# Kernel tuning notes

Measured on AMD Instinct MI355X. Metric: run time of the kernel, lower is better.

The kernel has to match this reference:

```python
import jax, jax.numpy as jnp
import numpy as np

B, S, D = 16, 2048, 512

def setup_inputs() -> dict:
    key = jax.random.key(0)
    k0, k1, k2, k3 = jax.random.split(key, 4)
    scale = 1.0 / np.sqrt(D)
    return {
        "inputs": jax.random.normal(k0, (B, S, D), dtype=jnp.float32),
        "W_q": jax.random.normal(k1, (D, D), dtype=jnp.float32) * scale,
        "W_k": jax.random.normal(k2, (D, D), dtype=jnp.float32) * scale,
        "W_v": jax.random.normal(k3, (D, D), dtype=jnp.float32) * scale,
    }

def reference(inputs, W_q, W_k, W_v):
    # Q/K/V projections: [B,S,D]
    q = jnp.einsum('bsd,de->bse', inputs, W_q)
    k = jnp.einsum('bsd,de->bse', inputs, W_k)
    v = jnp.einsum('bsd,de->bse', inputs, W_v)
    d_k = jnp.asarray(q.shape[-1], dtype=q.dtype)
    scores = jnp.einsum('bqd,bkd->bqk', q, k) / jnp.sqrt(d_k)  # [B,S,S]
    attn = jax.nn.softmax(scores, axis=-1)
    out = jnp.einsum('bqk,bkd->bqd', attn, v)  # [B,S,D]
    return jnp.sum(out, axis=1)  # sum-pool over seq -> [B,D]
```

## Files before the change

kernel.cpp:

```cpp
#include <hip/hip_runtime.h>
#include <hip/hip_bf16.h>


#define S_LEN 2048
#define D_DIM 512
#define BATCH 16

typedef short bf16x8 __attribute__((ext_vector_type(8)));
typedef float f32x4 __attribute__((ext_vector_type(4)));

typedef __attribute__((address_space(3))) void lds_void_t;
typedef const __attribute__((address_space(1))) void gbl_void_t;

__device__ __forceinline__ void async_copy16(const void* g, void* l) {
  __builtin_amdgcn_global_load_lds((gbl_void_t*)g, (lds_void_t*)l, 16, 0, 0);
}

__device__ __forceinline__ unsigned short f2bf(float f) {
  unsigned u = __float_as_uint(f);
  u += 0x7fff + ((u >> 16) & 1);
  return (unsigned short)(u >> 16);
}
__device__ __forceinline__ float bf2f(unsigned short h) {
  return __uint_as_float((unsigned)h << 16);
}

#if __has_builtin(__builtin_amdgcn_cvt_pk_fp8_f32) && __has_builtin(__builtin_amdgcn_cvt_f32_fp8)
#define HAVE_FP8CVT 1
#else
#define HAVE_FP8CVT 0
#endif

__device__ __forceinline__ unsigned enc8(float x) {
  unsigned u = __float_as_uint(x);
  unsigned t = (u + 0x7FFFFu + ((u >> 20) & 1u)) >> 20;
  int b = (int)t - 0x3C0;
  b = b < 0 ? 0 : (b > 127 ? 127 : b);
  return (unsigned)b;
}
__device__ __forceinline__ float dec8(unsigned b) {
  return b ? __uint_as_float((b + 0x3C0u) << 20) : 0.0f;
}

__device__ __forceinline__ unsigned pack4_fp8(float e0, float e1, float e2, float e3) {
#if HAVE_FP8CVT
  unsigned dw = (unsigned)__builtin_amdgcn_cvt_pk_fp8_f32(e0, e1, 0, false);
  dw = (unsigned)__builtin_amdgcn_cvt_pk_fp8_f32(e2, e3, (int)dw, true);
  return dw;
#else
  return enc8(e0) | (enc8(e1) << 8) | (enc8(e2) << 16) | (enc8(e3) << 24);
#endif
}

__device__ __forceinline__ void gemm_core_nt(
    const unsigned short* __restrict__ A, long lda,
    const unsigned short* __restrict__ B, long ldb,
    int K, unsigned short* As, unsigned short* Bs, f32x4 acc[4][4])
{
  const int tid  = threadIdx.x;
  const int lane = tid & 63;
  const int w    = tid >> 6;
  const int wm   = w >> 1, wn = w & 1;
  const int r16  = lane & 15;
  const int kq   = lane >> 4;

  const int j0 = w * 64 + lane;
  const int j1 = (w + 4) * 64 + lane;
  const int r0 = j0 >> 2, cc0 = (((j0 & 3) - (r0 >> 1)) & 3);
  const int r1 = j1 >> 2, cc1 = (((j1 & 3) - (r1 >> 1)) & 3);

  const long a0 = (long)r0 * lda + cc0 * 8;
  const long a1 = (long)r1 * lda + cc1 * 8;
  const long b0 = (long)r0 * ldb + cc0 * 8;
  const long b1 = (long)r1 * ldb + cc1 * 8;

  int aoff[4], boff[4];
#pragma unroll
  for (int mt = 0; mt < 4; ++mt) {
    const int row = wm * 64 + mt * 16 + r16;
    aoff[mt] = row * 32 + (((row >> 1) + kq) & 3) * 8;
  }
#pragma unroll
  for (int nt = 0; nt < 4; ++nt) {
    const int row = wn * 64 + nt * 16 + r16;
    boff[nt] = row * 32 + (((row >> 1) + kq) & 3) * 8;
  }

  for (int k0 = 0; k0 < K; k0 += 32) {
    __syncthreads();
    async_copy16(A + a0 + k0, (char*)As + (w    ) * 1024);
    async_copy16(A + a1 + k0, (char*)As + (w + 4) * 1024);
    async_copy16(B + b0 + k0, (char*)Bs + (w    ) * 1024);
    async_copy16(B + b1 + k0, (char*)Bs + (w + 4) * 1024);
    __syncthreads();

    bf16x8 af[4], bg[4];
#pragma unroll
    for (int mt = 0; mt < 4; ++mt) af[mt] = *(const bf16x8*)&As[aoff[mt]];
#pragma unroll
    for (int nt = 0; nt < 4; ++nt) bg[nt] = *(const bf16x8*)&Bs[boff[nt]];
#pragma unroll
    for (int mt = 0; mt < 4; ++mt)
#pragma unroll
      for (int nt = 0; nt < 4; ++nt)
        acc[mt][nt] = __builtin_amdgcn_mfma_f32_16x16x32_bf16(af[mt], bg[nt], acc[mt][nt], 0, 0, 0);
  }
}

__global__ __launch_bounds__(256) void k_prep(
    const float* __restrict__ X, const float* __restrict__ Wq, const float* __restrict__ Wk,
    unsigned short* __restrict__ Xbf, unsigned short* __restrict__ Wqb,
    unsigned short* __restrict__ Wkb, float* __restrict__ zp, float* __restrict__ out)
{
  const int blk = blockIdx.x;
  if (blk < 16384) {
    int i = (blk * 256 + threadIdx.x) * 4;
    float4 v = *(const float4*)(X + i);
    ushort4 o;
    o.x = f2bf(v.x); o.y = f2bf(v.y); o.z = f2bf(v.z); o.w = f2bf(v.w);
    *(ushort4*)(Xbf + i) = o;
  } else if (blk < 16896) {
    const int b2 = blk - 16384;
    const float* s = (b2 < 256) ? Wq : Wk;
    unsigned short* d = (b2 < 256) ? Wqb : Wkb;
    int i = ((b2 & 255) * 256 + threadIdx.x) * 4;
    float4 v = *(const float4*)(s + i);
    ushort4 o;
    o.x = f2bf(v.x); o.y = f2bf(v.y); o.z = f2bf(v.z); o.w = f2bf(v.w);
    *(ushort4*)(d + i) = o;
  } else {
    int i = (blk - 16896) * 256 + threadIdx.x;
    if (i < 73728) zp[i] = 0.0f;
    else out[i - 73728] = 0.0f;
  }
}

__global__ __launch_bounds__(256) void k_mt(
    const unsigned short* __restrict__ A, const unsigned short* __restrict__ B,
    unsigned short* __restrict__ C, float scale)
{
  __shared__ alignas(16) unsigned short As[64 * 32];
  __shared__ alignas(16) unsigned short Bs[64 * 32];
  f32x4 acc[2][2] = {};
  const int tid = threadIdx.x, lane = tid & 63, w = tid >> 6;
  const int wm = w >> 1, wn = w & 1, r16 = lane & 15, kq = lane >> 4;
  const long a0row = (long)blockIdx.y * 64, b0row = (long)blockIdx.x * 64;

  const int prow = tid >> 2, pslot = tid & 3, pc = (pslot - prow) & 3;
  const long asrc = (a0row + prow) * 512 + pc * 8;
  const long bsrc = (b0row + prow) * 512 + pc * 8;

  int aoff[2], boff[2];
#pragma unroll
  for (int t = 0; t < 2; ++t) {
    const int m = wm * 32 + t * 16 + r16;
    aoff[t] = m * 32 + ((m + kq) & 3) * 8;
    const int n = wn * 32 + t * 16 + r16;
    boff[t] = n * 32 + ((n + kq) & 3) * 8;
  }

  for (int k0 = 0; k0 < 512; k0 += 32) {
    __syncthreads();
    async_copy16(A + asrc + k0, (char*)As + w * 1024);
    async_copy16(B + bsrc + k0, (char*)Bs + w * 1024);
    __syncthreads();
    bf16x8 af[2], bg[2];
#pragma unroll
    for (int t = 0; t < 2; ++t) { af[t] = *(const bf16x8*)&As[aoff[t]]; bg[t] = *(const bf16x8*)&Bs[boff[t]]; }
#pragma unroll
    for (int mt = 0; mt < 2; ++mt)
#pragma unroll
      for (int nt = 0; nt < 2; ++nt)
        acc[mt][nt] = __builtin_amdgcn_mfma_f32_16x16x32_bf16(af[mt], bg[nt], acc[mt][nt], 0, 0, 0);
  }

  const int quad = lane >> 4;
#pragma unroll
  for (int mt = 0; mt < 2; ++mt)
#pragma unroll
    for (int nt = 0; nt < 2; ++nt)
#pragma unroll
      for (int r = 0; r < 4; ++r)
        C[(a0row + wm * 32 + mt * 16 + quad * 4 + r) * 512 + b0row + wn * 32 + nt * 16 + r16]
            = f2bf(acc[mt][nt][r] * scale);
}

__global__ __launch_bounds__(256) void k_gemm_bf16out(
    const unsigned short* __restrict__ A, long lda,
    const unsigned short* __restrict__ B, long ldb, int K,
    unsigned short* __restrict__ C, long ldc, float scale)
{
  __shared__ alignas(16) unsigned short As[128 * 32];
  __shared__ alignas(16) unsigned short Bs[128 * 32];
  f32x4 acc[4][4] = {};
  const long am0 = (long)blockIdx.y * 128;
  const long bn0 = (long)blockIdx.x * 128;
  gemm_core_nt(A + am0 * lda, lda, B + bn0 * ldb, ldb, K, As, Bs, acc);

  const int lane = threadIdx.x & 63;
  const int w = threadIdx.x >> 6, wm = w >> 1, wn = w & 1;
  const long row0 = am0 + wm * 64 + (lane >> 4) * 4;
  const long col0 = bn0 + wn * 64 + (lane & 15);
#pragma unroll
  for (int mt = 0; mt < 4; ++mt)
#pragma unroll
    for (int nt = 0; nt < 4; ++nt)
#pragma unroll
      for (int r = 0; r < 4; ++r)
        C[(row0 + mt * 16 + r) * ldc + col0 + nt * 16] = f2bf(acc[mt][nt][r] * scale);
}

union SMemAE {
  struct { unsigned short As[128 * 32]; unsigned short Bs[128 * 32]; } s;
  unsigned E32[128 * 36];
};

__global__ __launch_bounds__(256) void k_passAE(
    const unsigned short* __restrict__ Ybf, const unsigned short* __restrict__ Xbf,
    float* __restrict__ lrow, unsigned* __restrict__ E)
{
  __shared__ SMemAE sm;
  f32x4 acc[4][4] = {};
  const int b = blockIdx.z, qt = blockIdx.y, kt = blockIdx.x;
  const long q0 = (long)qt * 128;
  const long n0 = (long)kt * 128;
  gemm_core_nt(Ybf + ((long)b * S_LEN + q0) * D_DIM, D_DIM,
               Xbf + ((long)b * S_LEN + n0) * D_DIM, D_DIM, D_DIM,
               sm.s.As, sm.s.Bs, acc);

  const int lane = threadIdx.x & 63;
  const int w = threadIdx.x >> 6, wm = w >> 1, wn = w & 1;
  const int r16 = lane & 15, quad = lane >> 4;

  __syncthreads();

#pragma unroll
  for (int mt = 0; mt < 4; ++mt) {
    float rs[4] = {0.f, 0.f, 0.f, 0.f};
#pragma unroll
    for (int nt = 0; nt < 4; ++nt) {
      float ev[4];
#pragma unroll
      for (int r = 0; r < 4; ++r) {
        ev[r] = __builtin_amdgcn_exp2f(acc[mt][nt][r]);
        rs[r] += ev[r];
      }
      const int col = wn * 64 + nt * 16 + r16;
      const int r4  = wm * 16 + mt * 4 + quad;
      sm.E32[col * 36 + r4] = pack4_fp8(ev[0], ev[1], ev[2], ev[3]);
    }
#pragma unroll
    for (int r = 0; r < 4; ++r) {
      float s = rs[r];
      s += __shfl_xor(s, 1, 64);
      s += __shfl_xor(s, 2, 64);
      s += __shfl_xor(s, 4, 64);
      s += __shfl_xor(s, 8, 64);
      if (r16 == 0)
        atomicAdd(&lrow[(long)b * S_LEN + q0 + wm * 64 + mt * 16 + quad * 4 + r], s);
    }
  }
  __syncthreads();

  unsigned* Eg = E + (((long)(b * 16 + qt)) * 16 + kt) * 4096;
  const int t = threadIdx.x;
#pragma unroll
  for (int p = 0; p < 4; ++p) {
    const int n = p * 256 + t;
    const int col = n >> 3, hj = n & 7;
    uint4 v = *(const uint4*)&sm.E32[col * 36 + hj * 4];
    *(uint4*)(Eg + n * 4) = v;
  }
}

__global__ __launch_bounds__(256) void k_wsum(
    const unsigned* __restrict__ E, const float* __restrict__ lrow,
    float* __restrict__ wcol)
{
  __shared__ float rl[512];
  const int kt = blockIdx.x, qq = blockIdx.y, b = blockIdx.z;
  const int tid = threadIdx.x;
  {
    const float* lp = lrow + (long)b * S_LEN + qq * 512;
    rl[tid]       = 1.0f / lp[tid];
    rl[tid + 256] = 1.0f / lp[tid + 256];
  }
  __syncthreads();
  const int col = tid & 127, qsel = tid >> 7;
  float acc = 0.0f;
#pragma unroll
  for (int qt2 = 0; qt2 < 2; ++qt2) {
    const int qtl = qsel * 2 + qt2;
    const int qt = qq * 4 + qtl;
    const unsigned* Ep = E + (((long)(b * 16 + qt)) * 16 + kt) * 4096 + col * 32;
    const float* rlq = rl + qtl * 128;
#pragma unroll
    for (int j = 0; j < 8; ++j) {
      uint4 v = *(const uint4*)(Ep + j * 4);
      const unsigned dws[4] = {v.x, v.y, v.z, v.w};
#pragma unroll
      for (int i = 0; i < 4; ++i) {
        const unsigned dv = dws[i];
        const float* r = rlq + j * 16 + i * 4;
#if HAVE_FP8CVT
        acc += __builtin_amdgcn_cvt_f32_fp8((int)dv, 0) * r[0];
        acc += __builtin_amdgcn_cvt_f32_fp8((int)dv, 1) * r[1];
        acc += __builtin_amdgcn_cvt_f32_fp8((int)dv, 2) * r[2];
        acc += __builtin_amdgcn_cvt_f32_fp8((int)dv, 3) * r[3];
#else
        acc += dec8( dv        & 0xFFu) * r[0];
        acc += dec8((dv >>  8) & 0xFFu) * r[1];
        acc += dec8((dv >> 16) & 0xFFu) * r[2];
        acc += dec8((dv >> 24)        ) * r[3];
#endif
      }
    }
  }
  atomicAdd(&wcol[(long)b * S_LEN + kt * 128 + col], acc);
}

__global__ __launch_bounds__(256) void k_passA(
    const unsigned short* __restrict__ Ybf, const unsigned short* __restrict__ Xbf,
    float* __restrict__ lrow)
{
  __shared__ alignas(16) unsigned short As[128 * 32];
  __shared__ alignas(16) unsigned short Bs[128 * 32];
  f32x4 acc[4][4] = {};
  const int b = blockIdx.z;
  const long q0 = (long)blockIdx.y * 128;
  const long n0 = (long)blockIdx.x * 128;
  gemm_core_nt(Ybf + ((long)b * S_LEN + q0) * D_DIM, D_DIM,
               Xbf + ((long)b * S_LEN + n0) * D_DIM, D_DIM, D_DIM, As, Bs, acc);

  const int lane = threadIdx.x & 63;
  const int w = threadIdx.x >> 6, wm = w >> 1;
#pragma unroll
  for (int mt = 0; mt < 4; ++mt) {
#pragma unroll
    for (int r = 0; r < 4; ++r) {
      float s = 0.0f;
#pragma unroll
      for (int nt = 0; nt < 4; ++nt) s += __builtin_amdgcn_exp2f(acc[mt][nt][r]);
      s += __shfl_xor(s, 1, 64);
      s += __shfl_xor(s, 2, 64);
      s += __shfl_xor(s, 4, 64);
      s += __shfl_xor(s, 8, 64);
      if ((lane & 15) == 0)
        atomicAdd(&lrow[(long)b * S_LEN + q0 + wm * 64 + mt * 16 + (lane >> 4) * 4 + r], s);
    }
  }
}

__global__ __launch_bounds__(256) void k_passB(
    const unsigned short* __restrict__ Ybf, const unsigned short* __restrict__ Xbf,
    const float* __restrict__ lrow, float* __restrict__ wcol)
{
  __shared__ alignas(16) unsigned short As[128 * 32];
  __shared__ alignas(16) unsigned short Bs[128 * 32];
  f32x4 acc[4][4] = {};
  const int b = blockIdx.z;
  const long q0 = (long)blockIdx.y * 128;
  const long n0 = (long)blockIdx.x * 128;
  gemm_core_nt(Ybf + ((long)b * S_LEN + q0) * D_DIM, D_DIM,
               Xbf + ((long)b * S_LEN + n0) * D_DIM, D_DIM, D_DIM, As, Bs, acc);

  const int lane = threadIdx.x & 63;
  const int w = threadIdx.x >> 6, wm = w >> 1, wn = w & 1;
  float csv[4] = {0.0f, 0.0f, 0.0f, 0.0f};
#pragma unroll
  for (int mt = 0; mt < 4; ++mt) {
    const float4 lv = *(const float4*)&lrow[(long)b * S_LEN + q0 + wm * 64 + mt * 16 + (lane >> 4) * 4];
    const float rv[4] = {1.0f / lv.x, 1.0f / lv.y, 1.0f / lv.z, 1.0f / lv.w};
#pragma unroll
    for (int nt = 0; nt < 4; ++nt)
#pragma unroll
      for (int r = 0; r < 4; ++r)
        csv[nt] += __builtin_amdgcn_exp2f(acc[mt][nt][r]) * rv[r];
  }
#pragma unroll
  for (int nt = 0; nt < 4; ++nt) {
    csv[nt] += __shfl_xor(csv[nt], 16, 64);
    csv[nt] += __shfl_xor(csv[nt], 32, 64);
  }
  if (lane < 16) {
#pragma unroll
    for (int nt = 0; nt < 4; ++nt)
      atomicAdd(&wcol[(long)b * S_LEN + n0 + wn * 64 + nt * 16 + lane], csv[nt]);
  }
}

__global__ __launch_bounds__(256) void k_t(
    const unsigned short* __restrict__ Xbf, const float* __restrict__ wcol,
    float* __restrict__ tvec)
{
  const int b = blockIdx.z;
  const int d = blockIdx.x * 256 + threadIdx.x;
  const int k0 = blockIdx.y * 64;
  const unsigned short* Xp = Xbf + ((long)b * S_LEN + k0) * D_DIM + d;
  const float* wp = wcol + (long)b * S_LEN + k0;
  float acc = 0.0f;
#pragma unroll 8
  for (int k = 0; k < 64; ++k) acc += wp[k] * bf2f(Xp[(long)k * D_DIM]);
  atomicAdd(&tvec[b * D_DIM + d], acc);
}

__global__ __launch_bounds__(128) void k_out(
    const float* __restrict__ tvec, const float* __restrict__ Wv, float* __restrict__ out)
{
  __shared__ float tl[128];
  const int b = blockIdx.y;
  const int d0 = blockIdx.z * 128;
  const int e = blockIdx.x * 128 + threadIdx.x;
  tl[threadIdx.x] = tvec[b * D_DIM + d0 + threadIdx.x];
  __syncthreads();
  float acc = 0.0f;
#pragma unroll 8
  for (int d = 0; d < 128; ++d) acc += tl[d] * Wv[(long)(d0 + d) * D_DIM + e];
  atomicAdd(&out[b * D_DIM + e], acc);
}

extern "C" void kernel_launch(void* const* d_in, const int* in_sizes, int n_in,
                              void* d_out, int out_size, void* d_ws, size_t ws_size,
                              hipStream_t stream) {
  const float* X  = (const float*)d_in[0];
  const float* Wq = (const float*)d_in[1];
  const float* Wk = (const float*)d_in[2];
  const float* Wv = (const float*)d_in[3];
  float* out = (float*)d_out;

  char* ws = (char*)d_ws;
  unsigned short* Xbf = (unsigned short*)(ws);
  unsigned short* Ybf = (unsigned short*)(ws + 33554432);
  unsigned short* Mt  = (unsigned short*)(ws + 67108864);
  unsigned short* Wqb = (unsigned short*)(ws + 67633152);
  unsigned short* Wkb = (unsigned short*)(ws + 68157440);
  float* lrow = (float*)(ws + 68681728);
  float* wcol = (float*)(ws + 68812800);
  float* tvec = (float*)(ws + 68943872);
  unsigned* E = (unsigned*)(ws + 69206016);
  const bool bigws = ws_size >= (size_t)69206016 + (size_t)67108864;

  k_prep<<<17216, 256, 0, stream>>>(X, Wq, Wk, Xbf, Wqb, Wkb, lrow, out);

  const float scale = 1.4426950408889634f / 22.627416997969522f;
  k_mt<<<dim3(8, 8), 256, 0, stream>>>(Wkb, Wqb, Mt, scale);

  k_gemm_bf16out<<<dim3(4, 256), 256, 0, stream>>>(Xbf, 512, Mt, 512, 512, Ybf, 512, 1.0f);

  if (bigws) {
    k_passAE<<<dim3(16, 16, 16), 256, 0, stream>>>(Ybf, Xbf, lrow, E);
    k_wsum<<<dim3(16, 4, 16), 256, 0, stream>>>(E, lrow, wcol);
  } else {
    k_passA<<<dim3(16, 16, 16), 256, 0, stream>>>(Ybf, Xbf, lrow);
    k_passB<<<dim3(16, 16, 16), 256, 0, stream>>>(Ybf, Xbf, lrow, wcol);
  }

  k_t<<<dim3(2, 32, 16), 256, 0, stream>>>(Xbf, wcol, tvec);
  k_out<<<dim3(4, 16, 4), 128, 0, stream>>>(tvec, Wv, out);
}
```

Measured before the change: 272.3 us.

## Use 32x32x16 MFMA in score pass and replace tvec atomics with partials

The score GEMM in k_passAE moves from 16x16x32 MFMA tiles to 32x32x16 MFMA with a new LDS swizzle and fragment layout. The exp/row-sum epilogue is rewritten to match the 32x32 accumulator layout. This is meant to cut LDS fragment reads and instruction count per FLOP. Separately, k_t now writes per-chunk partial sums into a buffer that reuses the Ybf region, and k_out reduces them, which removes the float atomics and the tvec zeroing.

```diff
diff --git a/kernel.cpp b/kernel.cpp
--- a/kernel.cpp
+++ b/kernel.cpp
@@ -8,6 +8,7 @@
 
 typedef short bf16x8 __attribute__((ext_vector_type(8)));
 typedef float f32x4 __attribute__((ext_vector_type(4)));
+typedef float f32x16 __attribute__((ext_vector_type(16)));
 
 typedef __attribute__((address_space(3))) void lds_void_t;
 typedef const __attribute__((address_space(1))) void gbl_void_t;
@@ -104,6 +105,65 @@
 #pragma unroll
       for (int nt = 0; nt < 4; ++nt)
         acc[mt][nt] = __builtin_amdgcn_mfma_f32_16x16x32_bf16(af[mt], bg[nt], acc[mt][nt], 0, 0, 0);
+  }
+}
+
+__device__ __forceinline__ void gemm_core_nt32(
+    const unsigned short* __restrict__ A, long lda,
+    const unsigned short* __restrict__ B, long ldb,
+    int K, unsigned short* As, unsigned short* Bs, f32x16 acc2[2][2])
+{
+  const int tid  = threadIdx.x;
+  const int lane = tid & 63;
+  const int w    = tid >> 6;
+  const int wm   = w >> 1, wn = w & 1;
+  const int c32  = lane & 31;
+  const int g    = lane >> 5;
+
+  const int j0 = w * 64 + lane;
+  const int j1 = (w + 4) * 64 + lane;
+  const int r0 = j0 >> 2, cc0 = (((j0 & 3) - (r0 >> 1)) & 3);
+  const int r1 = j1 >> 2, cc1 = (((j1 & 3) - (r1 >> 1)) & 3);
+
+  const long a0 = (long)r0 * lda + cc0 * 8;
+  const long a1 = (long)r1 * lda + cc1 * 8;
+  const long b0 = (long)r0 * ldb + cc0 * 8;
+  const long b1 = (long)r1 * ldb + cc1 * 8;
+
+  int aoff[2][2], boff[2][2];
+#pragma unroll
+  for (int ks = 0; ks < 2; ++ks) {
+#pragma unroll
+    for (int t = 0; t < 2; ++t) {
+      const int m = wm * 64 + t * 32 + c32;
+      aoff[ks][t] = m * 32 + (((m >> 1) + ks * 2 + g) & 3) * 8;
+      const int n = wn * 64 + t * 32 + c32;
+      boff[ks][t] = n * 32 + (((n >> 1) + ks * 2 + g) & 3) * 8;
+    }
+  }
+
+  for (int k0 = 0; k0 < K; k0 += 32) {
+    __syncthreads();
+    async_copy16(A + a0 + k0, (char*)As + (w    ) * 1024);
+    async_copy16(A + a1 + k0, (char*)As + (w + 4) * 1024);
+    async_copy16(B + b0 + k0, (char*)Bs + (w    ) * 1024);
+    async_copy16(B + b1 + k0, (char*)Bs + (w + 4) * 1024);
+    __syncthreads();
+
+#pragma unroll
+    for (int ks = 0; ks < 2; ++ks) {
+      bf16x8 af[2], bg[2];
+#pragma unroll
+      for (int t = 0; t < 2; ++t) {
+        af[t] = *(const bf16x8*)&As[aoff[ks][t]];
+        bg[t] = *(const bf16x8*)&Bs[boff[ks][t]];
+      }
+#pragma unroll
+      for (int mt = 0; mt < 2; ++mt)
+#pragma unroll
+        for (int nt = 0; nt < 2; ++nt)
+          acc2[mt][nt] = __builtin_amdgcn_mfma_f32_32x32x16_bf16(af[mt], bg[nt], acc2[mt][nt], 0, 0, 0);
+    }
   }
 }
 
@@ -130,8 +190,8 @@
     *(ushort4*)(d + i) = o;
   } else {
     int i = (blk - 16896) * 256 + threadIdx.x;
-    if (i < 73728) zp[i] = 0.0f;
-    else out[i - 73728] = 0.0f;
+    if (i < 65536) zp[i] = 0.0f;
+    else out[i - 65536] = 0.0f;
   }
 }
 
@@ -220,44 +280,48 @@
     float* __restrict__ lrow, unsigned* __restrict__ E)
 {
   __shared__ SMemAE sm;
-  f32x4 acc[4][4] = {};
+  f32x16 acc2[2][2] = {};
   const int b = blockIdx.z, qt = blockIdx.y, kt = blockIdx.x;
   const long q0 = (long)qt * 128;
   const long n0 = (long)kt * 128;
-  gemm_core_nt(Ybf + ((long)b * S_LEN + q0) * D_DIM, D_DIM,
-               Xbf + ((long)b * S_LEN + n0) * D_DIM, D_DIM, D_DIM,
-               sm.s.As, sm.s.Bs, acc);
+  gemm_core_nt32(Ybf + ((long)b * S_LEN + q0) * D_DIM, D_DIM,
+                 Xbf + ((long)b * S_LEN + n0) * D_DIM, D_DIM, D_DIM,
+                 sm.s.As, sm.s.Bs, acc2);
 
   const int lane = threadIdx.x & 63;
   const int w = threadIdx.x >> 6, wm = w >> 1, wn = w & 1;
-  const int r16 = lane & 15, quad = lane >> 4;
+  const int c32 = lane & 31, g = lane >> 5;
 
   __syncthreads();
 
 #pragma unroll
-  for (int mt = 0; mt < 4; ++mt) {
-    float rs[4] = {0.f, 0.f, 0.f, 0.f};
-#pragma unroll
-    for (int nt = 0; nt < 4; ++nt) {
-      float ev[4];
+  for (int mt = 0; mt < 2; ++mt) {
+#pragma unroll
+    for (int j = 0; j < 4; ++j) {
+      float rs[4] = {0.f, 0.f, 0.f, 0.f};
+#pragma unroll
+      for (int nt = 0; nt < 2; ++nt) {
+        float ev[4];
+#pragma unroll
+        for (int r = 0; r < 4; ++r) {
+          ev[r] = __builtin_amdgcn_exp2f(acc2[mt][nt][j * 4 + r]);
+          rs[r] += ev[r];
+        }
+        const int col = wn * 64 + nt * 32 + c32;
+        const int r4  = wm * 16 + mt * 8 + j * 2 + g;
+        sm.E32[col * 36 + r4] = pack4_fp8(ev[0], ev[1], ev[2], ev[3]);
+      }
 #pragma unroll
       for (int r = 0; r < 4; ++r) {
-        ev[r] = __builtin_amdgcn_exp2f(acc[mt][nt][r]);
-        rs[r] += ev[r];
+        float s = rs[r];
+        s += __shfl_xor(s, 1, 64);
+        s += __shfl_xor(s, 2, 64);
+        s += __shfl_xor(s, 4, 64);
+        s += __shfl_xor(s, 8, 64);
+        s += __shfl_xor(s, 16, 64);
+        if (c32 == 0)
+          atomicAdd(&lrow[(long)b * S_LEN + q0 + wm * 64 + mt * 32 + j * 8 + g * 4 + r], s);
       }
-      const int col = wn * 64 + nt * 16 + r16;
-      const int r4  = wm * 16 + mt * 4 + quad;
-      sm.E32[col * 36 + r4] = pack4_fp8(ev[0], ev[1], ev[2], ev[3]);
-    }
-#pragma unroll
-    for (int r = 0; r < 4; ++r) {
-      float s = rs[r];
-      s += __shfl_xor(s, 1, 64);
-      s += __shfl_xor(s, 2, 64);
-      s += __shfl_xor(s, 4, 64);
-      s += __shfl_xor(s, 8, 64);
-      if (r16 == 0)
-        atomicAdd(&lrow[(long)b * S_LEN + q0 + wm * 64 + mt * 16 + quad * 4 + r], s);
     }
   }
   __syncthreads();
@@ -391,27 +455,31 @@
 
 __global__ __launch_bounds__(256) void k_t(
     const unsigned short* __restrict__ Xbf, const float* __restrict__ wcol,
-    float* __restrict__ tvec)
-{
-  const int b = blockIdx.z;
+    float* __restrict__ tpart)
+{
+  const int b = blockIdx.z, kc = blockIdx.y;
   const int d = blockIdx.x * 256 + threadIdx.x;
-  const int k0 = blockIdx.y * 64;
+  const int k0 = kc * 128;
   const unsigned short* Xp = Xbf + ((long)b * S_LEN + k0) * D_DIM + d;
   const float* wp = wcol + (long)b * S_LEN + k0;
   float acc = 0.0f;
 #pragma unroll 8
-  for (int k = 0; k < 64; ++k) acc += wp[k] * bf2f(Xp[(long)k * D_DIM]);
-  atomicAdd(&tvec[b * D_DIM + d], acc);
+  for (int k = 0; k < 128; ++k) acc += wp[k] * bf2f(Xp[(long)k * D_DIM]);
+  tpart[((long)kc * BATCH + b) * D_DIM + d] = acc;
 }
 
 __global__ __launch_bounds__(128) void k_out(
-    const float* __restrict__ tvec, const float* __restrict__ Wv, float* __restrict__ out)
+    const float* __restrict__ tpart, const float* __restrict__ Wv, float* __restrict__ out)
 {
   __shared__ float tl[128];
   const int b = blockIdx.y;
   const int d0 = blockIdx.z * 128;
   const int e = blockIdx.x * 128 + threadIdx.x;
-  tl[threadIdx.x] = tvec[b * D_DIM + d0 + threadIdx.x];
+  float tv = 0.0f;
+#pragma unroll
+  for (int kc = 0; kc < 16; ++kc)
+    tv += tpart[((long)kc * BATCH + b) * D_DIM + d0 + threadIdx.x];
+  tl[threadIdx.x] = tv;
   __syncthreads();
   float acc = 0.0f;
 #pragma unroll 8
@@ -436,11 +504,11 @@
   unsigned short* Wkb = (unsigned short*)(ws + 68157440);
   float* lrow = (float*)(ws + 68681728);
   float* wcol = (float*)(ws + 68812800);
-  float* tvec = (float*)(ws + 68943872);
   unsigned* E = (unsigned*)(ws + 69206016);
+  float* tpart = (float*)(ws + 33554432);
   const bool bigws = ws_size >= (size_t)69206016 + (size_t)67108864;
 
-  k_prep<<<17216, 256, 0, stream>>>(X, Wq, Wk, Xbf, Wqb, Wkb, lrow, out);
+  k_prep<<<17184, 256, 0, stream>>>(X, Wq, Wk, Xbf, Wqb, Wkb, lrow, out);
 
   const float scale = 1.4426950408889634f / 22.627416997969522f;
   k_mt<<<dim3(8, 8), 256, 0, stream>>>(Wkb, Wqb, Mt, scale);
@@ -455,6 +523,6 @@
     k_passB<<<dim3(16, 16, 16), 256, 0, stream>>>(Ybf, Xbf, lrow, wcol);
   }
 
-  k_t<<<dim3(2, 32, 16), 256, 0, stream>>>(Xbf, wcol, tvec);
-  k_out<<<dim3(4, 16, 4), 128, 0, stream>>>(tvec, Wv, out);
-}
+  k_t<<<dim3(2, 16, 16), 256, 0, stream>>>(Xbf, wcol, tpart);
+  k_out<<<dim3(4, 16, 4), 128, 0, stream>>>(tpart, Wv, out);
+}
```

After: 308.7 us. +13.4%, slower.

## Remap GEMM blocks per XCD for L2 locality and replace atomics with partial sums

Applied to the files above, without the earlier changes.

Block indices in the Y-projection GEMM and the scores pass are remapped so that consecutive blocks dispatched to the same XCD share a batch or row panel, which should improve L2 reuse on the chiplet design. The t-vector reduction no longer uses atomics: each block writes vectorized partial sums into a scratch buffer, and the output kernel reduces the 64 partials itself. The prep kernel stops zeroing the old tvec. The scratch buffer reuses the Ybf workspace region, which is safe only because Ybf is dead by that point in the stream.

```diff
diff --git a/kernel.cpp b/kernel.cpp
--- a/kernel.cpp
+++ b/kernel.cpp
@@ -130,8 +130,8 @@
     *(ushort4*)(d + i) = o;
   } else {
     int i = (blk - 16896) * 256 + threadIdx.x;
-    if (i < 73728) zp[i] = 0.0f;
-    else out[i - 73728] = 0.0f;
+    if (i < 65536) zp[i] = 0.0f;
+    else out[i - 65536] = 0.0f;
   }
 }
 
@@ -185,17 +185,18 @@
             = f2bf(acc[mt][nt][r] * scale);
 }
 
-__global__ __launch_bounds__(256) void k_gemm_bf16out(
-    const unsigned short* __restrict__ A, long lda,
-    const unsigned short* __restrict__ B, long ldb, int K,
-    unsigned short* __restrict__ C, long ldc, float scale)
+__global__ __launch_bounds__(256) void k_ygemm(
+    const unsigned short* __restrict__ A, const unsigned short* __restrict__ Mt,
+    unsigned short* __restrict__ C)
 {
   __shared__ alignas(16) unsigned short As[128 * 32];
   __shared__ alignas(16) unsigned short Bs[128 * 32];
   f32x4 acc[4][4] = {};
-  const long am0 = (long)blockIdx.y * 128;
-  const long bn0 = (long)blockIdx.x * 128;
-  gemm_core_nt(A + am0 * lda, lda, B + bn0 * ldb, ldb, K, As, Bs, acc);
+  const int L = blockIdx.x + (blockIdx.y << 2);
+  const int xcd = L & 7, seq = L >> 3;
+  const long am0 = (long)(xcd * 32 + (seq >> 2)) * 128;
+  const long bn0 = (long)(seq & 3) * 128;
+  gemm_core_nt(A + am0 * 512, 512, Mt + bn0 * 512, 512, 512, As, Bs, acc);
 
   const int lane = threadIdx.x & 63;
   const int w = threadIdx.x >> 6, wm = w >> 1, wn = w & 1;
@@ -207,7 +208,7 @@
     for (int nt = 0; nt < 4; ++nt)
 #pragma unroll
       for (int r = 0; r < 4; ++r)
-        C[(row0 + mt * 16 + r) * ldc + col0 + nt * 16] = f2bf(acc[mt][nt][r] * scale);
+        C[(row0 + mt * 16 + r) * 512 + col0 + nt * 16] = f2bf(acc[mt][nt][r]);
 }
 
 union SMemAE {
@@ -221,7 +222,11 @@
 {
   __shared__ SMemAE sm;
   f32x4 acc[4][4] = {};
-  const int b = blockIdx.z, qt = blockIdx.y, kt = blockIdx.x;
+  const int L = blockIdx.x + (blockIdx.y << 4) + (blockIdx.z << 8);
+  const int xcd = L & 7, seq = L >> 3;
+  const int b  = xcd * 2 + (seq >> 8);
+  const int s2 = seq & 255;
+  const int qt = s2 >> 4, kt = s2 & 15;
   const long q0 = (long)qt * 128;
   const long n0 = (long)kt * 128;
   gemm_core_nt(Ybf + ((long)b * S_LEN + q0) * D_DIM, D_DIM,
@@ -391,27 +396,39 @@
 
 __global__ __launch_bounds__(256) void k_t(
     const unsigned short* __restrict__ Xbf, const float* __restrict__ wcol,
-    float* __restrict__ tvec)
-{
-  const int b = blockIdx.z;
-  const int d = blockIdx.x * 256 + threadIdx.x;
-  const int k0 = blockIdx.y * 64;
+    float* __restrict__ tpart)
+{
+  const int b = blockIdx.z, kc = blockIdx.y;
+  const int tid = threadIdx.x;
+  const int c4 = tid & 127, ksel = tid >> 7;
+  const int k0 = kc * 64 + ksel * 32;
+  const int d = c4 * 4;
   const unsigned short* Xp = Xbf + ((long)b * S_LEN + k0) * D_DIM + d;
   const float* wp = wcol + (long)b * S_LEN + k0;
-  float acc = 0.0f;
+  float a0 = 0, a1 = 0, a2 = 0, a3 = 0;
 #pragma unroll 8
-  for (int k = 0; k < 64; ++k) acc += wp[k] * bf2f(Xp[(long)k * D_DIM]);
-  atomicAdd(&tvec[b * D_DIM + d], acc);
+  for (int k = 0; k < 32; ++k) {
+    ushort4 xv = *(const ushort4*)(Xp + (long)k * D_DIM);
+    const float wv = wp[k];
+    a0 += wv * bf2f(xv.x); a1 += wv * bf2f(xv.y);
+    a2 += wv * bf2f(xv.z); a3 += wv * bf2f(xv.w);
+  }
+  float4 o; o.x = a0; o.y = a1; o.z = a2; o.w = a3;
+  *(float4*)&tpart[((long)(kc * 2 + ksel) * BATCH + b) * D_DIM + d] = o;
 }
 
 __global__ __launch_bounds__(128) void k_out(
-    const float* __restrict__ tvec, const float* __restrict__ Wv, float* __restrict__ out)
+    const float* __restrict__ tpart, const float* __restrict__ Wv, float* __restrict__ out)
 {
   __shared__ float tl[128];
   const int b = blockIdx.y;
   const int d0 = blockIdx.z * 128;
   const int e = blockIdx.x * 128 + threadIdx.x;
-  tl[threadIdx.x] = tvec[b * D_DIM + d0 + threadIdx.x];
+  float tv = 0.0f;
+#pragma unroll
+  for (int p = 0; p < 64; ++p)
+    tv += tpart[((long)p * BATCH + b) * D_DIM + d0 + threadIdx.x];
+  tl[threadIdx.x] = tv;
   __syncthreads();
   float acc = 0.0f;
 #pragma unroll 8
@@ -436,16 +453,16 @@
   unsigned short* Wkb = (unsigned short*)(ws + 68157440);
   float* lrow = (float*)(ws + 68681728);
   float* wcol = (float*)(ws + 68812800);
-  float* tvec = (float*)(ws + 68943872);
   unsigned* E = (unsigned*)(ws + 69206016);
+  float* tpart = (float*)(ws + 33554432);
   const bool bigws = ws_size >= (size_t)69206016 + (size_t)67108864;
 
-  k_prep<<<17216, 256, 0, stream>>>(X, Wq, Wk, Xbf, Wqb, Wkb, lrow, out);
+  k_prep<<<17184, 256, 0, stream>>>(X, Wq, Wk, Xbf, Wqb, Wkb, lrow, out);
 
   const float scale = 1.4426950408889634f / 22.627416997969522f;
   k_mt<<<dim3(8, 8), 256, 0, stream>>>(Wkb, Wqb, Mt, scale);
 
-  k_gemm_bf16out<<<dim3(4, 256), 256, 0, stream>>>(Xbf, 512, Mt, 512, 512, Ybf, 512, 1.0f);
+  k_ygemm<<<dim3(4, 256), 256, 0, stream>>>(Xbf, Mt, Ybf);
 
   if (bigws) {
     k_passAE<<<dim3(16, 16, 16), 256, 0, stream>>>(Ybf, Xbf, lrow, E);
@@ -455,6 +472,6 @@
     k_passB<<<dim3(16, 16, 16), 256, 0, stream>>>(Ybf, Xbf, lrow, wcol);
   }
 
-  k_t<<<dim3(2, 32, 16), 256, 0, stream>>>(Xbf, wcol, tvec);
-  k_out<<<dim3(4, 16, 4), 128, 0, stream>>>(tvec, Wv, out);
-}
+  k_t<<<dim3(1, 32, 16), 256, 0, stream>>>(Xbf, wcol, tpart);
+  k_out<<<dim3(4, 16, 4), 128, 0, stream>>>(tpart, Wv, out);
+}
```

New measurement: 309.5 us. +13.7%, slower.

## Compute attention score GEMM in FP8 using scaled MFMA 16x16x128

Applied to the files above, without the earlier changes.

Adds an FP8 path for the dominant score GEMM (Y·X^T per batch). X is packed to FP8 during the prep kernel and Y is cast to FP8 by a new kernel, then a new k_passAE_f8 kernel uses the mfma_scale 16x16x128 f8f6f4 instruction with K-tiles of 128. The softmax scale moves from the Mt GEMM epilogue into the exp2 argument so the projected Y keeps magnitudes that suit FP8. This is meant to roughly halve the operand traffic and raise matrix throughput, at the cost of an extra cast pass over Y, a larger workspace and lower score precision. The path only runs when the workspace is large enough, and the small-workspace fallback now also writes E past the old size check.

```diff
diff --git a/kernel.cpp b/kernel.cpp
--- a/kernel.cpp
+++ b/kernel.cpp
@@ -8,9 +8,12 @@
 
 typedef short bf16x8 __attribute__((ext_vector_type(8)));
 typedef float f32x4 __attribute__((ext_vector_type(4)));
+typedef int i32x8 __attribute__((ext_vector_type(8)));
 
 typedef __attribute__((address_space(3))) void lds_void_t;
 typedef const __attribute__((address_space(1))) void gbl_void_t;
+
+#define KSCL 0.06376281516217733f
 
 __device__ __forceinline__ void async_copy16(const void* g, void* l) {
   __builtin_amdgcn_global_load_lds((gbl_void_t*)g, (lds_void_t*)l, 16, 0, 0);
@@ -25,31 +28,10 @@
   return __uint_as_float((unsigned)h << 16);
 }
 
-#if __has_builtin(__builtin_amdgcn_cvt_pk_fp8_f32) && __has_builtin(__builtin_amdgcn_cvt_f32_fp8)
-#define HAVE_FP8CVT 1
-#else
-#define HAVE_FP8CVT 0
-#endif
-
-__device__ __forceinline__ unsigned enc8(float x) {
-  unsigned u = __float_as_uint(x);
-  unsigned t = (u + 0x7FFFFu + ((u >> 20) & 1u)) >> 20;
-  int b = (int)t - 0x3C0;
-  b = b < 0 ? 0 : (b > 127 ? 127 : b);
-  return (unsigned)b;
-}
-__device__ __forceinline__ float dec8(unsigned b) {
-  return b ? __uint_as_float((b + 0x3C0u) << 20) : 0.0f;
-}
-
 __device__ __forceinline__ unsigned pack4_fp8(float e0, float e1, float e2, float e3) {
-#if HAVE_FP8CVT
   unsigned dw = (unsigned)__builtin_amdgcn_cvt_pk_fp8_f32(e0, e1, 0, false);
   dw = (unsigned)__builtin_amdgcn_cvt_pk_fp8_f32(e2, e3, (int)dw, true);
   return dw;
-#else
-  return enc8(e0) | (enc8(e1) << 8) | (enc8(e2) << 16) | (enc8(e3) << 24);
-#endif
 }
 
 __device__ __forceinline__ void gemm_core_nt(
@@ -109,8 +91,9 @@
 
 __global__ __launch_bounds__(256) void k_prep(
     const float* __restrict__ X, const float* __restrict__ Wq, const float* __restrict__ Wk,
-    unsigned short* __restrict__ Xbf, unsigned short* __restrict__ Wqb,
-    unsigned short* __restrict__ Wkb, float* __restrict__ zp, float* __restrict__ out)
+    unsigned short* __restrict__ Xbf, unsigned* __restrict__ Xf8,
+    unsigned short* __restrict__ Wqb, unsigned short* __restrict__ Wkb,
+    float* __restrict__ zp, float* __restrict__ out)
 {
   const int blk = blockIdx.x;
   if (blk < 16384) {
@@ -119,6 +102,7 @@
     ushort4 o;
     o.x = f2bf(v.x); o.y = f2bf(v.y); o.z = f2bf(v.z); o.w = f2bf(v.w);
     *(ushort4*)(Xbf + i) = o;
+    if (Xf8) Xf8[blk * 256 + threadIdx.x] = pack4_fp8(v.x, v.y, v.z, v.w);
   } else if (blk < 16896) {
     const int b2 = blk - 16384;
     const float* s = (b2 < 256) ? Wq : Wk;
@@ -135,9 +119,17 @@
   }
 }
 
+__global__ __launch_bounds__(256) void k_casty(
+    const unsigned short* __restrict__ Ybf, unsigned* __restrict__ Yf8)
+{
+  const int i = blockIdx.x * 256 + threadIdx.x;
+  ushort4 v = *(const ushort4*)(Ybf + (long)i * 4);
+  Yf8[i] = pack4_fp8(bf2f(v.x), bf2f(v.y), bf2f(v.z), bf2f(v.w));
+}
+
 __global__ __launch_bounds__(256) void k_mt(
     const unsigned short* __restrict__ A, const unsigned short* __restrict__ B,
-    unsigned short* __restrict__ C, float scale)
+    unsigned short* __restrict__ C)
 {
   __shared__ alignas(16) unsigned short As[64 * 32];
   __shared__ alignas(16) unsigned short Bs[64 * 32];
@@ -182,13 +174,13 @@
 #pragma unroll
       for (int r = 0; r < 4; ++r)
         C[(a0row + wm * 32 + mt * 16 + quad * 4 + r) * 512 + b0row + wn * 32 + nt * 16 + r16]
-            = f2bf(acc[mt][nt][r] * scale);
+            = f2bf(acc[mt][nt][r]);
 }
 
 __global__ __launch_bounds__(256) void k_gemm_bf16out(
     const unsigned short* __restrict__ A, long lda,
     const unsigned short* __restrict__ B, long ldb, int K,
-    unsigned short* __restrict__ C, long ldc, float scale)
+    unsigned short* __restrict__ C, long ldc)
 {
   __shared__ alignas(16) unsigned short As[128 * 32];
   __shared__ alignas(16) unsigned short Bs[128 * 32];
@@ -207,7 +199,121 @@
     for (int nt = 0; nt < 4; ++nt)
 #pragma unroll
       for (int r = 0; r < 4; ++r)
-        C[(row0 + mt * 16 + r) * ldc + col0 + nt * 16] = f2bf(acc[mt][nt][r] * scale);
+        C[(row0 + mt * 16 + r) * ldc + col0 + nt * 16] = f2bf(acc[mt][nt][r]);
+}
+
+union SMemF8 {
+  struct { unsigned char As[128 * 128]; unsigned char Bs[128 * 128]; } s;
+  unsigned E32[128 * 36];
+};
+
+__global__ __launch_bounds__(256) void k_passAE_f8(
+    const unsigned* __restrict__ Yf8, const unsigned* __restrict__ Xf8,
+    float* __restrict__ lrow, unsigned* __restrict__ E)
+{
+  __shared__ SMemF8 sm;
+  f32x4 acc[4][4] = {};
+  const int b = blockIdx.z, qt = blockIdx.y, kt = blockIdx.x;
+  const long q0 = (long)qt * 128;
+  const long n0 = (long)kt * 128;
+  const unsigned char* A = (const unsigned char*)Yf8 + ((long)b * S_LEN + q0) * D_DIM;
+  const unsigned char* B = (const unsigned char*)Xf8 + ((long)b * S_LEN + n0) * D_DIM;
+
+  const int tid  = threadIdx.x;
+  const int lane = tid & 63;
+  const int w    = tid >> 6;
+  const int wm   = w >> 1, wn = w & 1;
+  const int r16  = lane & 15;
+  const int quad = lane >> 4;
+
+  long gsrc[4];
+#pragma unroll
+  for (int p = 0; p < 4; ++p) {
+    const int j = p * 256 + tid;
+    const int row = j >> 3, slot = j & 7, c = (slot - row) & 7;
+    gsrc[p] = (long)row * 512 + c * 16;
+  }
+
+  int aoff[4][2], boff[4][2];
+#pragma unroll
+  for (int t = 0; t < 4; ++t) {
+#pragma unroll
+    for (int h = 0; h < 2; ++h) {
+      const int m = wm * 64 + t * 16 + r16;
+      aoff[t][h] = m * 128 + ((quad * 2 + h + m) & 7) * 16;
+      const int n = wn * 64 + t * 16 + r16;
+      boff[t][h] = n * 128 + ((quad * 2 + h + n) & 7) * 16;
+    }
+  }
+
+  for (int k0 = 0; k0 < 512; k0 += 128) {
+    __syncthreads();
+#pragma unroll
+    for (int p = 0; p < 4; ++p) {
+      async_copy16(A + gsrc[p] + k0, sm.s.As + (p * 256 + tid - lane) * 16);
+      async_copy16(B + gsrc[p] + k0, sm.s.Bs + (p * 256 + tid - lane) * 16);
+    }
+    __syncthreads();
+
+    i32x8 af[4], bg[4];
+#pragma unroll
+    for (int t = 0; t < 4; ++t) {
+      uint4 lo = *(const uint4*)&sm.s.As[aoff[t][0]];
+      uint4 hi = *(const uint4*)&sm.s.As[aoff[t][1]];
+      af[t][0] = lo.x; af[t][1] = lo.y; af[t][2] = lo.z; af[t][3] = lo.w;
+      af[t][4] = hi.x; af[t][5] = hi.y; af[t][6] = hi.z; af[t][7] = hi.w;
+      uint4 blo = *(const uint4*)&sm.s.Bs[boff[t][0]];
+      uint4 bhi = *(const uint4*)&sm.s.Bs[boff[t][1]];
+      bg[t][0] = blo.x; bg[t][1] = blo.y; bg[t][2] = blo.z; bg[t][3] = blo.w;
+      bg[t][4] = bhi.x; bg[t][5] = bhi.y; bg[t][6] = bhi.z; bg[t][7] = bhi.w;
+    }
+#pragma unroll
+    for (int mt = 0; mt < 4; ++mt)
+#pragma unroll
+      for (int nt = 0; nt < 4; ++nt)
+        acc[mt][nt] = __builtin_amdgcn_mfma_scale_f32_16x16x128_f8f6f4(
+            af[mt], bg[nt], acc[mt][nt], 0, 0,
+            0, 0x7F7F7F7F, 0, 0x7F7F7F7F);
+  }
+
+  __syncthreads();
+
+#pragma unroll
+  for (int mt = 0; mt < 4; ++mt) {
+    float rs[4] = {0.f, 0.f, 0.f, 0.f};
+#pragma unroll
+    for (int nt = 0; nt < 4; ++nt) {
+      float ev[4];
+#pragma unroll
+      for (int r = 0; r < 4; ++r) {
+        ev[r] = __builtin_amdgcn_exp2f(acc[mt][nt][r] * KSCL);
+        rs[r] += ev[r];
+      }
+      const int col = wn * 64 + nt * 16 + r16;
+      const int r4  = wm * 16 + mt * 4 + quad;
+      sm.E32[col * 36 + r4] = pack4_fp8(ev[0], ev[1], ev[2], ev[3]);
+    }
+#pragma unroll
+    for (int r = 0; r < 4; ++r) {
+      float s = rs[r];
+      s += __shfl_xor(s, 1, 64);
+      s += __shfl_xor(s, 2, 64);
+      s += __shfl_xor(s, 4, 64);
+      s += __shfl_xor(s, 8, 64);
+      if (r16 == 0)
+        atomicAdd(&lrow[(long)b * S_LEN + q0 + wm * 64 + mt * 16 + quad * 4 + r], s);
+    }
+  }
+  __syncthreads();
+
+  unsigned* Eg = E + (((long)(b * 16 + qt)) * 16 + kt) * 4096;
+#pragma unroll
+  for (int p = 0; p < 4; ++p) {
+    const int n = p * 256 + tid;
+    const int col = n >> 3, hj = n & 7;
+    uint4 v = *(const uint4*)&sm.E32[col * 36 + hj * 4];
+    *(uint4*)(Eg + n * 4) = v;
+  }
 }
 
 union SMemAE {
@@ -242,7 +348,7 @@
       float ev[4];
 #pragma unroll
       for (int r = 0; r < 4; ++r) {
-        ev[r] = __builtin_amdgcn_exp2f(acc[mt][nt][r]);
+        ev[r] = __builtin_amdgcn_exp2f(acc[mt][nt][r] * KSCL);
         rs[r] += ev[r];
       }
       const int col = wn * 64 + nt * 16 + r16;
@@ -302,91 +408,14 @@
       for (int i = 0; i < 4; ++i) {
         const unsigned dv = dws[i];
         const float* r = rlq + j * 16 + i * 4;
-#if HAVE_FP8CVT
         acc += __builtin_amdgcn_cvt_f32_fp8((int)dv, 0) * r[0];
         acc += __builtin_amdgcn_cvt_f32_fp8((int)dv, 1) * r[1];
         acc += __builtin_amdgcn_cvt_f32_fp8((int)dv, 2) * r[2];
         acc += __builtin_amdgcn_cvt_f32_fp8((int)dv, 3) * r[3];
-#else
-        acc += dec8( dv        & 0xFFu) * r[0];
-        acc += dec8((dv >>  8) & 0xFFu) * r[1];
-        acc += dec8((dv >> 16) & 0xFFu) * r[2];
-        acc += dec8((dv >> 24)        ) * r[3];
-#endif
       }
     }
   }
   atomicAdd(&wcol[(long)b * S_LEN + kt * 128 + col], acc);
-}
-
-__global__ __launch_bounds__(256) void k_passA(
-    const unsigned short* __restrict__ Ybf, const unsigned short* __restrict__ Xbf,
-    float* __restrict__ lrow)
-{
-  __shared__ alignas(16) unsigned short As[128 * 32];
-  __shared__ alignas(16) unsigned short Bs[128 * 32];
-  f32x4 acc[4][4] = {};
-  const int b = blockIdx.z;
-  const long q0 = (long)blockIdx.y * 128;
-  const long n0 = (long)blockIdx.x * 128;
-  gemm_core_nt(Ybf + ((long)b * S_LEN + q0) * D_DIM, D_DIM,
-               Xbf + ((long)b * S_LEN + n0) * D_DIM, D_DIM, D_DIM, As, Bs, acc);
-
-  const int lane = threadIdx.x & 63;
-  const int w = threadIdx.x >> 6, wm = w >> 1;
-#pragma unroll
-  for (int mt = 0; mt < 4; ++mt) {
-#pragma unroll
-    for (int r = 0; r < 4; ++r) {
-      float s = 0.0f;
-#pragma unroll
-      for (int nt = 0; nt < 4; ++nt) s += __builtin_amdgcn_exp2f(acc[mt][nt][r]);
-      s += __shfl_xor(s, 1, 64);
-      s += __shfl_xor(s, 2, 64);
-      s += __shfl_xor(s, 4, 64);
-      s += __shfl_xor(s, 8, 64);
-      if ((lane & 15) == 0)
-        atomicAdd(&lrow[(long)b * S_LEN + q0 + wm * 64 + mt * 16 + (lane >> 4) * 4 + r], s);
-    }
-  }
-}
-
-__global__ __launch_bounds__(256) void k_passB(
-    const unsigned short* __restrict__ Ybf, const unsigned short* __restrict__ Xbf,
-    const float* __restrict__ lrow, float* __restrict__ wcol)
-{
-  __shared__ alignas(16) unsigned short As[128 * 32];
-  __shared__ alignas(16) unsigned short Bs[128 * 32];
-  f32x4 acc[4][4] = {};
-  const int b = blockIdx.z;
-  const long q0 = (long)blockIdx.y * 128;
-  const long n0 = (long)blockIdx.x * 128;
-  gemm_core_nt(Ybf + ((long)b * S_LEN + q0) * D_DIM, D_DIM,
-               Xbf + ((long)b * S_LEN + n0) * D_DIM, D_DIM, D_DIM, As, Bs, acc);
-
-  const int lane = threadIdx.x & 63;
-  const int w = threadIdx.x >> 6, wm = w >> 1, wn = w & 1;
-  float csv[4] = {0.0f, 0.0f, 0.0f, 0.0f};
-#pragma unroll
-  for (int mt = 0; mt < 4; ++mt) {
-    const float4 lv = *(const float4*)&lrow[(long)b * S_LEN + q0 + wm * 64 + mt * 16 + (lane >> 4) * 4];
-    const float rv[4] = {1.0f / lv.x, 1.0f / lv.y, 1.0f / lv.z, 1.0f / lv.w};
-#pragma unroll
-    for (int nt = 0; nt < 4; ++nt)
-#pragma unroll
-      for (int r = 0; r < 4; ++r)
-        csv[nt] += __builtin_amdgcn_exp2f(acc[mt][nt][r]) * rv[r];
-  }
-#pragma unroll
-  for (int nt = 0; nt < 4; ++nt) {
-    csv[nt] += __shfl_xor(csv[nt], 16, 64);
-    csv[nt] += __shfl_xor(csv[nt], 32, 64);
-  }
-  if (lane < 16) {
-#pragma unroll
-    for (int nt = 0; nt < 4; ++nt)
-      atomicAdd(&wcol[(long)b * S_LEN + n0 + wn * 64 + nt * 16 + lane], csv[nt]);
-  }
 }
 
 __global__ __launch_bounds__(256) void k_t(
@@ -437,22 +466,29 @@
   float* lrow = (float*)(ws + 68681728);
   float* wcol = (float*)(ws + 68812800);
   float* tvec = (float*)(ws + 68943872);
-  unsigned* E = (unsigned*)(ws + 69206016);
-  const bool bigws = ws_size >= (size_t)69206016 + (size_t)67108864;
-
-  k_prep<<<17216, 256, 0, stream>>>(X, Wq, Wk, Xbf, Wqb, Wkb, lrow, out);
-
-  const float scale = 1.4426950408889634f / 22.627416997969522f;
-  k_mt<<<dim3(8, 8), 256, 0, stream>>>(Wkb, Wqb, Mt, scale);
-
-  k_gemm_bf16out<<<dim3(4, 256), 256, 0, stream>>>(Xbf, 512, Mt, 512, 512, Ybf, 512, 1.0f);
-
-  if (bigws) {
+  unsigned* E   = (unsigned*)(ws + 69206016);
+  unsigned* Xf8 = (unsigned*)(ws + 136314880);
+  unsigned* Yf8 = (unsigned*)(ws + 153092096);
+  const bool bigws  = ws_size >= (size_t)136314880;
+  const bool f8path = ws_size >= (size_t)169869312;
+
+  k_prep<<<17216, 256, 0, stream>>>(X, Wq, Wk, Xbf, f8path ? Xf8 : nullptr,
+                                    Wqb, Wkb, lrow, out);
+
+  k_mt<<<dim3(8, 8), 256, 0, stream>>>(Wkb, Wqb, Mt);
+
+  k_gemm_bf16out<<<dim3(4, 256), 256, 0, stream>>>(Xbf, 512, Mt, 512, 512, Ybf, 512);
+
+  if (f8path) {
+    k_casty<<<16384, 256, 0, stream>>>(Ybf, Yf8);
+    k_passAE_f8<<<dim3(16, 16, 16), 256, 0, stream>>>(Yf8, Xf8, lrow, E);
+    k_wsum<<<dim3(16, 4, 16), 256, 0, stream>>>(E, lrow, wcol);
+  } else if (bigws) {
     k_passAE<<<dim3(16, 16, 16), 256, 0, stream>>>(Ybf, Xbf, lrow, E);
     k_wsum<<<dim3(16, 4, 16), 256, 0, stream>>>(E, lrow, wcol);
   } else {
-    k_passA<<<dim3(16, 16, 16), 256, 0, stream>>>(Ybf, Xbf, lrow);
-    k_passB<<<dim3(16, 16, 16), 256, 0, stream>>>(Ybf, Xbf, lrow, wcol);
+    k_passAE<<<dim3(16, 16, 16), 256, 0, stream>>>(Ybf, Xbf, lrow, E);
+    k_wsum<<<dim3(16, 4, 16), 256, 0, stream>>>(E, lrow, wcol);
   }
 
   k_t<<<dim3(2, 32, 16), 256, 0, stream>>>(Xbf, wcol, tvec);
```

Result: slower. 336.1 us (+23.4%).
